# Kernel tuning notes

Hardware: AMD Instinct MI355X
Metric: run time of the kernel (lower is better)

## Reference

```python
import jax, jax.numpy as jnp
import numpy as np

N, E, D_IN, D, H = 50000, 600000, 128, 128, 128
NEG_SLOPE = 0.2  # PyG GATConv default


def setup_inputs() -> dict:
    key = jax.random.key(0)
    ks = jax.random.split(key, 10)
    s = 1.0 / np.sqrt(D)
    return {
        "x": jax.random.normal(ks[0], (N, D_IN), jnp.float32),
        "edge_index": jax.random.randint(ks[1], (2, E), 0, N, jnp.int64),
        "h": jax.random.normal(ks[2], (1, N, H), jnp.float32),
        "c": jax.random.normal(ks[3], (1, N, H), jnp.float32),
        "W": jax.random.normal(ks[4], (D_IN, D), jnp.float32) * s,
        "att_src": jax.random.normal(ks[5], (D,), jnp.float32) * s,
        "att_dst": jax.random.normal(ks[6], (D,), jnp.float32) * s,
        "bias_gat": jnp.zeros((D,), jnp.float32),
        "W_ih": jax.random.normal(ks[7], (4 * H, D), jnp.float32) * s,
        "W_hh": jax.random.normal(ks[8], (4 * H, H), jnp.float32) * s,
    }


def _gat_conv(x, edge_index, W, att_src, att_dst, bias_gat):
    n = x.shape[0]
    xs = x @ W  # [N, D]
    # add self loops (PyG default add_self_loops=True)
    loop = jnp.arange(n, dtype=edge_index.dtype)
    src = jnp.concatenate([edge_index[0], loop])
    dst = jnp.concatenate([edge_index[1], loop])
    a_src = xs @ att_src  # [N]
    a_dst = xs @ att_dst  # [N]
    e = a_src[src] + a_dst[dst]  # [E+N]
    e = jnp.where(e >= 0, e, NEG_SLOPE * e)  # leaky_relu
    # segment softmax over edges grouped by destination node
    e_max = jax.ops.segment_max(e, dst, num_segments=n)
    e_exp = jnp.exp(e - e_max[dst])
    e_sum = jax.ops.segment_sum(e_exp, dst, num_segments=n)
    alpha = e_exp / (e_sum[dst] + 1e-16)  # [E+N]
    out = jax.ops.segment_sum(alpha[:, None] * xs[src], dst, num_segments=n)
    return out + bias_gat


def _lstm_step(x, h0, c0, W_ih, W_hh):
    # torch LSTM gate order: i, f, g, o; bias=False
    gates = x @ W_ih.T + h0 @ W_hh.T  # [N, 4H]
    i, f, g, o = jnp.split(gates, 4, axis=-1)
    i, f, o = jax.nn.sigmoid(i), jax.nn.sigmoid(f), jax.nn.sigmoid(o)
    g = jnp.tanh(g)
    c1 = f * c0 + i * g
    h1 = o * jnp.tanh(c1)
    return h1, c1


def reference(x, edge_index, h, c, W, att_src, att_dst, bias_gat, W_ih, W_hh):
    xb = jnp.tanh(_gat_conv(x, edge_index, W, att_src, att_dst, bias_gat))  # [N, D]
    h1, c1 = _lstm_step(xb, h[0], c[0], W_ih, W_hh)
    # LSTM output for seq_len=1 equals the new hidden state
    return xb * 0 + h1, h1[None], c1[None]
```

## Files before the change

kernel.cpp:

```cpp
#include <hip/hip_runtime.h>
#include <hip/hip_bf16.h>
#include <math.h>

#define NEG 0.2f

typedef float f32x4 __attribute__((ext_vector_type(4)));
typedef short bf16x8 __attribute__((ext_vector_type(8)));

__device__ __forceinline__ float fsig(float x){ return 1.0f/(1.0f+__expf(-x)); }
__device__ __forceinline__ float ftanh(float x){ float e = __expf(2.0f*x); return 1.0f - 2.0f/(e+1.0f); }
__device__ __forceinline__ unsigned short f2bf(float v){
    __hip_bfloat16 b = __float2bfloat16(v);
    return *(unsigned short*)&b;
}
__device__ __forceinline__ bf16x8 pack8(float4 u, float4 v){
    bf16x8 r;
    r[0]=(short)f2bf(u.x); r[1]=(short)f2bf(u.y); r[2]=(short)f2bf(u.z); r[3]=(short)f2bf(u.w);
    r[4]=(short)f2bf(v.x); r[5]=(short)f2bf(v.y); r[6]=(short)f2bf(v.z); r[7]=(short)f2bf(v.w);
    return r;
}

__global__ __launch_bounds__(256) void k_pack(const float* __restrict__ W,
                                              const float* __restrict__ W_ih,
                                              const float* __restrict__ W_hh,
                                              unsigned short* __restrict__ WPX,
                                              unsigned short* __restrict__ WP2){
    const int bid = blockIdx.x;
    if(bid < 8){
        int f = bid*256 + threadIdx.x;
        int l = f&63, ct = (f>>6)&7, ks = f>>9;
        int k0 = ks*32 + (l>>4)*8;
        int col = ct*16 + (l&15);
        #pragma unroll
        for(int j=0;j<8;j++) WPX[(size_t)f*8+j] = f2bf(W[(size_t)(k0+j)*128 + col]);
    } else {
        int f = (bid-8)*256 + threadIdx.x;
        int l = f&63, ct = (f>>6)&3, ks = (f>>8)&7, g = f>>11;
        int k0 = ks*32 + (l>>4)*8;
        int col = ct*128 + g*16 + (l&15);
        #pragma unroll
        for(int j=0;j<8;j++){
            int k = k0+j;
            float w = (k<128) ? W_ih[(size_t)col*128+k] : W_hh[(size_t)col*128+(k-128)];
            WP2[(size_t)f*8+j] = f2bf(w);
        }
    }
}

__global__ __launch_bounds__(256,2) void k_gemm_xs3(const float* __restrict__ x,
                                                    const unsigned short* __restrict__ WPX,
                                                    const float* __restrict__ att_s,
                                                    const float* __restrict__ att_d,
                                                    unsigned short* __restrict__ xsb,
                                                    float* __restrict__ a_src,
                                                    float* __restrict__ a_dst,
                                                    int n, int ntiles, int nwaves){
    const int w = threadIdx.x>>6, l = threadIdx.x&63;
    const int wid = blockIdx.x*4 + w;
    bf16x8 B[32];
    #pragma unroll
    for(int f=0;f<32;f++) B[f] = *(const bf16x8*)(WPX + (size_t)(f*64 + l)*8);
    float asv[8], adv[8];
    #pragma unroll
    for(int ct=0;ct<8;ct++){
        asv[ct] = att_s[ct*16 + (l&15)];
        adv[ct] = att_d[ct*16 + (l&15)];
    }
    for(int rt = wid; rt < ntiles; rt += nwaves){
        int arow = rt*16 + (l&15); if(arow>=n) arow = n-1;
        const float* xr = x + (size_t)arow*128 + (l>>4)*8;
        bf16x8 A[4];
        #pragma unroll
        for(int ks=0;ks<4;ks++){
            float4 u = *(const float4*)(xr + ks*32);
            float4 v = *(const float4*)(xr + ks*32 + 4);
            A[ks] = pack8(u,v);
        }
        f32x4 acc[8];
        #pragma unroll
        for(int ct=0;ct<8;ct++) acc[ct] = (f32x4){0.f,0.f,0.f,0.f};
        #pragma unroll
        for(int ks=0;ks<4;ks++){
            #pragma unroll
            for(int ct=0;ct<8;ct++)
                acc[ct] = __builtin_amdgcn_mfma_f32_16x16x32_bf16(A[ks], B[ks*8+ct], acc[ct], 0,0,0);
        }
        #pragma unroll
        for(int reg=0;reg<4;reg++){
            int row = rt*16 + (l>>4)*4 + reg;
            float ps=0.f, pd=0.f;
            #pragma unroll
            for(int ct=0;ct<8;ct++){ ps += acc[ct][reg]*asv[ct]; pd += acc[ct][reg]*adv[ct]; }
            ps += __shfl_xor(ps,1); pd += __shfl_xor(pd,1);
            ps += __shfl_xor(ps,2); pd += __shfl_xor(pd,2);
            ps += __shfl_xor(ps,4); pd += __shfl_xor(pd,4);
            ps += __shfl_xor(ps,8); pd += __shfl_xor(pd,8);
            if((l&15)==0 && row<n){ a_src[row]=ps; a_dst[row]=pd; }
            if(row<n){
                #pragma unroll
                for(int ct=0;ct<8;ct++)
                    xsb[(size_t)row*128 + ct*16 + (l&15)] = f2bf(acc[ct][reg]);
            }
        }
    }
}

__global__ __launch_bounds__(256) void k_hist(const int* __restrict__ ei,
                                              int* __restrict__ deg, int E, int EN){
    const int l = threadIdx.x & 63;
    unsigned long long m = __ballot(ei[2*l+1] != 0);
    const bool i64 = (m == 0ULL);
    int e = blockIdx.x*256 + threadIdx.x;
    if(e>=EN) return;
    int dst = (e>=E) ? (e-E) : (i64 ? ei[2*(size_t)(E+e)] : ei[(size_t)E+e]);
    atomicAdd(&deg[dst], 1);
}

__global__ __launch_bounds__(256) void k_scan1(const int* __restrict__ deg,
                                               int* __restrict__ bsum, int n){
    __shared__ int ws[4];
    int b = blockIdx.x, t = threadIdx.x;
    int i = b*512 + t*2;
    int s = 0;
    if(i<n)   s += deg[i];
    if(i+1<n) s += deg[i+1];
    for(int off=32;off;off>>=1) s += __shfl_xor(s,off);
    if((t&63)==0) ws[t>>6]=s;
    __syncthreads();
    if(t==0) bsum[b]=ws[0]+ws[1]+ws[2]+ws[3];
}

__global__ __launch_bounds__(256) void k_scan3(const int* __restrict__ deg,
                                               const int* __restrict__ bsum,
                                               int* __restrict__ rowptr,
                                               int* __restrict__ cursor,
                                               int n, int EN){
    __shared__ int wsum[4];
    __shared__ int boff;
    int b = blockIdx.x, t = threadIdx.x;
    if(t < 64){
        int a = 0;
        for(int i=t; i<b; i+=64) a += bsum[i];
        for(int off=32;off;off>>=1) a += __shfl_xor(a,off);
        if(t==0) boff = a;
    }
    int i = b*512 + t*2;
    int d0 = (i<n)?deg[i]:0, d1 = (i+1<n)?deg[i+1]:0;
    int s = d0+d1;
    int x = s;
    int lane = t&63, wv = t>>6;
    for(int dd=1; dd<64; dd<<=1){ int y=__shfl_up(x,dd); if(lane>=dd) x+=y; }
    if(lane==63) wsum[wv]=x;
    __syncthreads();
    int woff=0;
    for(int w=0;w<wv;w++) woff += wsum[w];
    int ex = boff + woff + x - s;
    if(i<n)   { rowptr[i]  =ex;    cursor[i]  =ex;    }
    if(i+1<n) { rowptr[i+1]=ex+d0; cursor[i+1]=ex+d0; }
    if(b==0 && t==0) rowptr[n]=EN;
}

__global__ __launch_bounds__(256) void k_fill(const int* __restrict__ ei,
                                              int* __restrict__ cursor,
                                              int* __restrict__ csr_src, int E, int EN){
    const int l = threadIdx.x & 63;
    unsigned long long m = __ballot(ei[2*l+1] != 0);
    const bool i64 = (m == 0ULL);
    int e = blockIdx.x*256 + threadIdx.x;
    if(e>=EN) return;
    int src,dst;
    if(e>=E){ src=dst=e-E; }
    else if(i64){ src = ei[2*(size_t)e]; dst = ei[2*(size_t)(E+e)]; }
    else        { src = ei[(size_t)e];   dst = ei[(size_t)E+e]; }
    int pos = atomicAdd(&cursor[dst], 1);
    csr_src[pos] = src;
}

__global__ __launch_bounds__(256) void k_agg3(const int* __restrict__ rowptr,
                                              const int* __restrict__ csr_src,
                                              const float* __restrict__ a_src,
                                              const float* __restrict__ a_dst,
                                              const unsigned int* __restrict__ xsb32,
                                              const float* __restrict__ bg,
                                              const float* __restrict__ h0,
                                              unsigned short* __restrict__ xh, int n){
    const int wv = threadIdx.x>>6, l = threadIdx.x&63;
    const int dst = blockIdx.x*4 + wv;
    if(dst>=n) return;
    const int beg = rowptr[dst], end = rowptr[dst+1];
    const float ad = a_dst[dst];
    float ax=0.f, ay=0.f, psum=0.f;
    int j = beg;
    for(; j+8<=end; j+=8){
        int s0=csr_src[j],   s1=csr_src[j+1], s2=csr_src[j+2], s3=csr_src[j+3];
        int s4=csr_src[j+4], s5=csr_src[j+5], s6=csr_src[j+6], s7=csr_src[j+7];
        float e0=a_src[s0]+ad, e1=a_src[s1]+ad, e2=a_src[s2]+ad, e3=a_src[s3]+ad;
        float e4=a_src[s4]+ad, e5=a_src[s5]+ad, e6=a_src[s6]+ad, e7=a_src[s7]+ad;
        unsigned k0=xsb32[(size_t)s0*64+l], k1=xsb32[(size_t)s1*64+l];
        unsigned k2=xsb32[(size_t)s2*64+l], k3=xsb32[(size_t)s3*64+l];
        unsigned k4=xsb32[(size_t)s4*64+l], k5=xsb32[(size_t)s5*64+l];
        unsigned k6=xsb32[(size_t)s6*64+l], k7=xsb32[(size_t)s7*64+l];
        e0=e0>=0.f?e0:NEG*e0; e1=e1>=0.f?e1:NEG*e1; e2=e2>=0.f?e2:NEG*e2; e3=e3>=0.f?e3:NEG*e3;
        e4=e4>=0.f?e4:NEG*e4; e5=e5>=0.f?e5:NEG*e5; e6=e6>=0.f?e6:NEG*e6; e7=e7>=0.f?e7:NEG*e7;
        float p0=__expf(e0), p1=__expf(e1), p2=__expf(e2), p3=__expf(e3);
        float p4=__expf(e4), p5=__expf(e5), p6=__expf(e6), p7=__expf(e7);
        psum += (p0+p1+p2+p3)+(p4+p5+p6+p7);
        ax += p0*__uint_as_float(k0<<16) + p1*__uint_as_float(k1<<16)
            + p2*__uint_as_float(k2<<16) + p3*__uint_as_float(k3<<16)
            + p4*__uint_as_float(k4<<16) + p5*__uint_as_float(k5<<16)
            + p6*__uint_as_float(k6<<16) + p7*__uint_as_float(k7<<16);
        ay += p0*__uint_as_float(k0&0xffff0000u) + p1*__uint_as_float(k1&0xffff0000u)
            + p2*__uint_as_float(k2&0xffff0000u) + p3*__uint_as_float(k3&0xffff0000u)
            + p4*__uint_as_float(k4&0xffff0000u) + p5*__uint_as_float(k5&0xffff0000u)
            + p6*__uint_as_float(k6&0xffff0000u) + p7*__uint_as_float(k7&0xffff0000u);
    }
    for(; j<end; ++j){
        int s = csr_src[j];
        float sv = a_src[s]+ad;
        sv = sv>=0.f ? sv : NEG*sv;
        float p = __expf(sv);
        psum += p;
        unsigned pk = xsb32[(size_t)s*64 + l];
        ax += p*__uint_as_float(pk<<16);
        ay += p*__uint_as_float(pk & 0xffff0000u);
    }
    const float inv = 1.0f/(psum + 1e-16f);
    float t0 = ftanh(ax*inv + bg[2*l]);
    float t1 = ftanh(ay*inv + bg[2*l+1]);
    unsigned int pk = (unsigned)f2bf(t0) | ((unsigned)f2bf(t1)<<16);
    unsigned int* xr = (unsigned int*)(xh + (size_t)dst*256);
    xr[l] = pk;
    float2 hv = *(const float2*)(h0 + (size_t)dst*128 + 2*l);
    xr[64 + l] = (unsigned)f2bf(hv.x) | ((unsigned)f2bf(hv.y)<<16);
}

__global__ __launch_bounds__(256,4) void k_lstm11(const unsigned short* __restrict__ xh,
                                                  const unsigned short* __restrict__ WP2,
                                                  const float* __restrict__ c0,
                                                  float* __restrict__ out,
                                                  int n, int ntiles){
    __shared__ unsigned short Bl[16384];
    const int t = threadIdx.x;
    const int w = t>>6, l = t&63;
    const int half = blockIdx.x & 1;
    const int rt = (blockIdx.x>>1)*4 + w;
    const bool live = (rt < ntiles);
    const size_t nn = (size_t)n*128;
    bf16x8 A[8];
    if(live){
        int arow = rt*16 + (l&15); if(arow>=n) arow=n-1;
        const unsigned short* ar = xh + (size_t)arow*256 + (l>>4)*8;
        #pragma unroll
        for(int ks=0;ks<8;ks++) A[ks] = *(const bf16x8*)(ar + ks*32);
    }
    const int rbase = rt*16 + (l>>4)*4;
    float cc[4][4];
    if(live){
        #pragma unroll
        for(int gi=0;gi<4;gi++){
            int col = (half*4+gi)*16 + (l&15);
            #pragma unroll
            for(int r=0;r<4;r++){ int rr=rbase+r; if(rr>=n) rr=n-1; cc[gi][r]=c0[(size_t)rr*128+col]; }
        }
    }
    #pragma unroll
    for(int gi=0; gi<4; ++gi){
        const int g = half*4 + gi;
        __syncthreads();
        {
            const float4* gsrc = (const float4*)(WP2 + (size_t)g*16384);
            float4* ldst = (float4*)Bl;
            #pragma unroll
            for(int i=0;i<8;i++) ldst[t + i*256] = gsrc[t + i*256];
        }
        __syncthreads();
        if(!live) continue;
        const int col = g*16 + (l&15);
        f32x4 acc[4];
        #pragma unroll
        for(int ct=0;ct<4;ct++) acc[ct] = (f32x4){0.f,0.f,0.f,0.f};
        #pragma unroll
        for(int ks=0;ks<8;ks++){
            #pragma unroll
            for(int ct=0;ct<4;ct++){
                const bf16x8 b = *(const bf16x8*)(Bl + ((ks*4+ct)*64 + l)*8);
                acc[ct] = __builtin_amdgcn_mfma_f32_16x16x32_bf16(A[ks], b, acc[ct], 0,0,0);
            }
        }
        #pragma unroll
        for(int reg=0;reg<4;reg++){
            int row = rbase + reg;
            if(row>=n) continue;
            float gi_=acc[0][reg], gf=acc[1][reg], gg=acc[2][reg], go=acc[3][reg];
            float c1v = fsig(gf)*cc[gi][reg] + fsig(gi_)*ftanh(gg);
            float h1v = fsig(go)*ftanh(c1v);
            out[(size_t)row*128+col]        = h1v;
            out[nn + (size_t)row*128+col]   = h1v;
            out[2*nn + (size_t)row*128+col] = c1v;
        }
    }
}

extern "C" void kernel_launch(void* const* d_in, const int* in_sizes, int n_in,
                              void* d_out, int out_size, void* d_ws, size_t ws_size,
                              hipStream_t stream) {
    const float* x      = (const float*)d_in[0];
    const int*   ei     = (const int*)  d_in[1];
    const float* h      = (const float*)d_in[2];
    const float* c      = (const float*)d_in[3];
    const float* W      = (const float*)d_in[4];
    const float* atts   = (const float*)d_in[5];
    const float* attd   = (const float*)d_in[6];
    const float* bias   = (const float*)d_in[7];
    const float* W_ih   = (const float*)d_in[8];
    const float* W_hh   = (const float*)d_in[9];
    float* out = (float*)d_out;

    const int n  = in_sizes[0]/128;
    const int E  = in_sizes[1]/2;
    const int EN = E + n;
    const int NB = (n + 511)/512;
    const int ntiles = (n + 15)/16;
    const int n2 = ntiles*16;

    unsigned short* xsb = (unsigned short*)d_ws;
    unsigned short* xh  = xsb + (size_t)n*128;
    unsigned short* WP2 = xh + (size_t)n2*256;
    unsigned short* WPX = WP2 + 131072;
    float* a_src = (float*)(WPX + 16384);
    float* a_dst = a_src + n;
    int*   deg    = (int*)(a_dst + n);
    int*   rowptr = deg + n;
    int*   cursor = rowptr + n + 1;
    int*   bsum   = cursor + n;
    int*   csr_src= bsum + 128;

    hipMemsetAsync(deg, 0, (size_t)n*sizeof(int), stream);
    k_pack<<<72,256,0,stream>>>(W, W_ih, W_hh, WPX, WP2);
    k_gemm_xs3<<<1024,256,0,stream>>>(x, WPX, atts, attd, xsb, a_src, a_dst, n, ntiles, 4096);
    k_hist<<<(EN+255)/256,256,0,stream>>>(ei,deg,E,EN);
    k_scan1<<<NB,256,0,stream>>>(deg,bsum,n);
    k_scan3<<<NB,256,0,stream>>>(deg,bsum,rowptr,cursor,n,EN);
    k_fill<<<(EN+255)/256,256,0,stream>>>(ei,cursor,csr_src,E,EN);
    k_agg3<<<(n+3)/4,256,0,stream>>>(rowptr,csr_src,a_src,a_dst,(const unsigned int*)xsb,bias,h,xh,n);
    k_lstm11<<<2*((ntiles+3)/4),256,0,stream>>>(xh, WP2, c, out, n, ntiles);
}
```

Measured before the change: 168.1 us.

## Fuse degree memset and histogram into existing kernels; register-resident persistent LSTM GEMM

The degree array is now zeroed inside the weight-pack kernel instead of by a separate memset. The edge histogram runs as extra blocks of the xs GEMM kernel, which removes two launches. The LSTM kernel becomes persistent: each wave keeps one gate group's weight slice in registers, loops over row tiles and prefetches the next tile's A and c0. This drops the LDS staging and the per-gate __syncthreads. In exchange it uses more registers (occupancy 2), and each wave reloads A for one column group, so A is re-read across 8 waves.

```diff
diff --git a/kernel.cpp b/kernel.cpp
--- a/kernel.cpp
+++ b/kernel.cpp
@@ -19,12 +19,14 @@
     r[4]=(short)f2bf(v.x); r[5]=(short)f2bf(v.y); r[6]=(short)f2bf(v.z); r[7]=(short)f2bf(v.w);
     return r;
 }
+__device__ __forceinline__ bf16x8 asbf(f32x4 v){ union{f32x4 f; bf16x8 h;} u; u.f=v; return u.h; }
 
 __global__ __launch_bounds__(256) void k_pack(const float* __restrict__ W,
                                               const float* __restrict__ W_ih,
                                               const float* __restrict__ W_hh,
                                               unsigned short* __restrict__ WPX,
-                                              unsigned short* __restrict__ WP2){
+                                              unsigned short* __restrict__ WP2,
+                                              int* __restrict__ deg, int n){
     const int bid = blockIdx.x;
     if(bid < 8){
         int f = bid*256 + threadIdx.x;
@@ -33,7 +35,7 @@
         int col = ct*16 + (l&15);
         #pragma unroll
         for(int j=0;j<8;j++) WPX[(size_t)f*8+j] = f2bf(W[(size_t)(k0+j)*128 + col]);
-    } else {
+    } else if(bid < 72){
         int f = (bid-8)*256 + threadIdx.x;
         int l = f&63, ct = (f>>6)&3, ks = (f>>8)&7, g = f>>11;
         int k0 = ks*32 + (l>>4)*8;
@@ -44,19 +46,36 @@
             float w = (k<128) ? W_ih[(size_t)col*128+k] : W_hh[(size_t)col*128+(k-128)];
             WP2[(size_t)f*8+j] = f2bf(w);
         }
-    }
-}
-
-__global__ __launch_bounds__(256,2) void k_gemm_xs3(const float* __restrict__ x,
-                                                    const unsigned short* __restrict__ WPX,
-                                                    const float* __restrict__ att_s,
-                                                    const float* __restrict__ att_d,
-                                                    unsigned short* __restrict__ xsb,
-                                                    float* __restrict__ a_src,
-                                                    float* __restrict__ a_dst,
-                                                    int n, int ntiles, int nwaves){
+    } else {
+        int i = (bid-72)*256 + threadIdx.x;
+        if(i < n) deg[i] = 0;
+    }
+}
+
+__global__ __launch_bounds__(256,2) void k_gemm_hist(const float* __restrict__ x,
+                                                     const unsigned short* __restrict__ WPX,
+                                                     const float* __restrict__ att_s,
+                                                     const float* __restrict__ att_d,
+                                                     unsigned short* __restrict__ xsb,
+                                                     float* __restrict__ a_src,
+                                                     float* __restrict__ a_dst,
+                                                     const int* __restrict__ ei,
+                                                     int* __restrict__ deg,
+                                                     int n, int ntiles, int gemmBlk,
+                                                     int E, int EN){
+    if((int)blockIdx.x >= gemmBlk){
+        const int l = threadIdx.x & 63;
+        unsigned long long m = __ballot(ei[2*l+1] != 0);
+        const bool i64 = (m == 0ULL);
+        int e = (blockIdx.x - gemmBlk)*256 + threadIdx.x;
+        if(e>=EN) return;
+        int dst = (e>=E) ? (e-E) : (i64 ? ei[2*(size_t)(E+e)] : ei[(size_t)E+e]);
+        atomicAdd(&deg[dst], 1);
+        return;
+    }
     const int w = threadIdx.x>>6, l = threadIdx.x&63;
     const int wid = blockIdx.x*4 + w;
+    const int nwaves = gemmBlk*4;
     bf16x8 B[32];
     #pragma unroll
     for(int f=0;f<32;f++) B[f] = *(const bf16x8*)(WPX + (size_t)(f*64 + l)*8);
@@ -103,17 +122,6 @@
             }
         }
     }
-}
-
-__global__ __launch_bounds__(256) void k_hist(const int* __restrict__ ei,
-                                              int* __restrict__ deg, int E, int EN){
-    const int l = threadIdx.x & 63;
-    unsigned long long m = __ballot(ei[2*l+1] != 0);
-    const bool i64 = (m == 0ULL);
-    int e = blockIdx.x*256 + threadIdx.x;
-    if(e>=EN) return;
-    int dst = (e>=E) ? (e-E) : (i64 ? ei[2*(size_t)(E+e)] : ei[(size_t)E+e]);
-    atomicAdd(&deg[dst], 1);
 }
 
 __global__ __launch_bounds__(256) void k_scan1(const int* __restrict__ deg,
@@ -234,69 +242,73 @@
     xr[64 + l] = (unsigned)f2bf(hv.x) | ((unsigned)f2bf(hv.y)<<16);
 }
 
-__global__ __launch_bounds__(256,4) void k_lstm11(const unsigned short* __restrict__ xh,
-                                                  const unsigned short* __restrict__ WP2,
-                                                  const float* __restrict__ c0,
-                                                  float* __restrict__ out,
-                                                  int n, int ntiles){
-    __shared__ unsigned short Bl[16384];
+__global__ __launch_bounds__(256,2) void k_lstm7(const unsigned short* __restrict__ xh,
+                                                 const unsigned short* __restrict__ WP2,
+                                                 const float* __restrict__ c0,
+                                                 float* __restrict__ out,
+                                                 int n, int ntiles, int wstride){
     const int t = threadIdx.x;
     const int w = t>>6, l = t&63;
-    const int half = blockIdx.x & 1;
-    const int rt = (blockIdx.x>>1)*4 + w;
-    const bool live = (rt < ntiles);
+    const int wid = blockIdx.x*4 + w;
+    const int g = wid & 7, wgi = wid >> 3;
+    const unsigned short* wp = WP2 + (size_t)g*16384;
+    f32x4 B[32];
+    #pragma unroll
+    for(int f=0;f<32;f++) B[f] = *(const f32x4*)(wp + (size_t)(f*64 + l)*8);
+    #pragma unroll
+    for(int f=0;f<32;f++) asm volatile("" : "+v"(B[f]));
     const size_t nn = (size_t)n*128;
-    bf16x8 A[8];
-    if(live){
+    const int col = g*16 + (l&15);
+    int rt = wgi;
+    if(rt >= ntiles) return;
+    bf16x8 A[8]; float cc[4];
+    {
         int arow = rt*16 + (l&15); if(arow>=n) arow=n-1;
         const unsigned short* ar = xh + (size_t)arow*256 + (l>>4)*8;
         #pragma unroll
         for(int ks=0;ks<8;ks++) A[ks] = *(const bf16x8*)(ar + ks*32);
-    }
-    const int rbase = rt*16 + (l>>4)*4;
-    float cc[4][4];
-    if(live){
-        #pragma unroll
-        for(int gi=0;gi<4;gi++){
-            int col = (half*4+gi)*16 + (l&15);
-            #pragma unroll
-            for(int r=0;r<4;r++){ int rr=rbase+r; if(rr>=n) rr=n-1; cc[gi][r]=c0[(size_t)rr*128+col]; }
-        }
-    }
-    #pragma unroll
-    for(int gi=0; gi<4; ++gi){
-        const int g = half*4 + gi;
-        __syncthreads();
-        {
-            const float4* gsrc = (const float4*)(WP2 + (size_t)g*16384);
-            float4* ldst = (float4*)Bl;
-            #pragma unroll
-            for(int i=0;i<8;i++) ldst[t + i*256] = gsrc[t + i*256];
-        }
-        __syncthreads();
-        if(!live) continue;
-        const int col = g*16 + (l&15);
+        int rbase = rt*16 + (l>>4)*4;
+        #pragma unroll
+        for(int r=0;r<4;r++){ int rr=rbase+r; if(rr>=n) rr=n-1; cc[r]=c0[(size_t)rr*128+col]; }
+    }
+    while(rt < ntiles){
+        const int rtn = rt + wstride;
+        bf16x8 A2[8]; float cc2[4];
+        if(rtn < ntiles){
+            int arow = rtn*16 + (l&15); if(arow>=n) arow=n-1;
+            const unsigned short* ar = xh + (size_t)arow*256 + (l>>4)*8;
+            #pragma unroll
+            for(int ks=0;ks<8;ks++) A2[ks] = *(const bf16x8*)(ar + ks*32);
+            int rbase = rtn*16 + (l>>4)*4;
+            #pragma unroll
+            for(int r=0;r<4;r++){ int rr=rbase+r; if(rr>=n) rr=n-1; cc2[r]=c0[(size_t)rr*128+col]; }
+        }
         f32x4 acc[4];
         #pragma unroll
         for(int ct=0;ct<4;ct++) acc[ct] = (f32x4){0.f,0.f,0.f,0.f};
         #pragma unroll
         for(int ks=0;ks<8;ks++){
             #pragma unroll
-            for(int ct=0;ct<4;ct++){
-                const bf16x8 b = *(const bf16x8*)(Bl + ((ks*4+ct)*64 + l)*8);
-                acc[ct] = __builtin_amdgcn_mfma_f32_16x16x32_bf16(A[ks], b, acc[ct], 0,0,0);
-            }
+            for(int ct=0;ct<4;ct++)
+                acc[ct] = __builtin_amdgcn_mfma_f32_16x16x32_bf16(A[ks], asbf(B[ks*4+ct]), acc[ct], 0,0,0);
         }
         #pragma unroll
         for(int reg=0;reg<4;reg++){
-            int row = rbase + reg;
+            int row = rt*16 + (l>>4)*4 + reg;
             if(row>=n) continue;
-            float gi_=acc[0][reg], gf=acc[1][reg], gg=acc[2][reg], go=acc[3][reg];
-            float c1v = fsig(gf)*cc[gi][reg] + fsig(gi_)*ftanh(gg);
+            float gi=acc[0][reg], gf=acc[1][reg], gg=acc[2][reg], go=acc[3][reg];
+            float c1v = fsig(gf)*cc[reg] + fsig(gi)*ftanh(gg);
             float h1v = fsig(go)*ftanh(c1v);
             out[(size_t)row*128+col]        = h1v;
             out[nn + (size_t)row*128+col]   = h1v;
             out[2*nn + (size_t)row*128+col] = c1v;
+        }
+        rt = rtn;
+        if(rt < ntiles){
+            #pragma unroll
+            for(int ks=0;ks<8;ks++) A[ks] = A2[ks];
+            #pragma unroll
+            for(int r=0;r<4;r++) cc[r] = cc2[r];
         }
     }
 }
@@ -322,6 +334,8 @@
     const int NB = (n + 511)/512;
     const int ntiles = (n + 15)/16;
     const int n2 = ntiles*16;
+    const int histBlk = (EN + 255)/256;
+    const int degBlk  = (n + 255)/256;
 
     unsigned short* xsb = (unsigned short*)d_ws;
     unsigned short* xh  = xsb + (size_t)n*128;
@@ -335,13 +349,12 @@
     int*   bsum   = cursor + n;
     int*   csr_src= bsum + 128;
 
-    hipMemsetAsync(deg, 0, (size_t)n*sizeof(int), stream);
-    k_pack<<<72,256,0,stream>>>(W, W_ih, W_hh, WPX, WP2);
-    k_gemm_xs3<<<1024,256,0,stream>>>(x, WPX, atts, attd, xsb, a_src, a_dst, n, ntiles, 4096);
-    k_hist<<<(EN+255)/256,256,0,stream>>>(ei,deg,E,EN);
+    k_pack<<<72+degBlk,256,0,stream>>>(W, W_ih, W_hh, WPX, WP2, deg, n);
+    k_gemm_hist<<<1024+histBlk,256,0,stream>>>(x, WPX, atts, attd, xsb, a_src, a_dst,
+                                               ei, deg, n, ntiles, 1024, E, EN);
     k_scan1<<<NB,256,0,stream>>>(deg,bsum,n);
     k_scan3<<<NB,256,0,stream>>>(deg,bsum,rowptr,cursor,n,EN);
-    k_fill<<<(EN+255)/256,256,0,stream>>>(ei,cursor,csr_src,E,EN);
+    k_fill<<<histBlk,256,0,stream>>>(ei,cursor,csr_src,E,EN);
     k_agg3<<<(n+3)/4,256,0,stream>>>(rowptr,csr_src,a_src,a_dst,(const unsigned int*)xsb,bias,h,xh,n);
-    k_lstm11<<<2*((ntiles+3)/4),256,0,stream>>>(xh, WP2, c, out, n, ntiles);
-}
+    k_lstm7<<<1024,256,0,stream>>>(xh, WP2, c, out, n, ntiles, 512);
+}
```

Result: no change. 167.0 us (-0.6%).
